# Performance work log

Hardware: AMD Instinct MI355X
Metric: run time of the kernel (lower is better)

The kernel has to match this reference:

```python
import jax, jax.numpy as jnp
import numpy as np

B, S, D = 4, 2048, 1024
H, DH = 16, 64  # dim_q = dim_k = D // H
DFF = 4096


def setup_inputs() -> dict:
    key = jax.random.key(0)
    ks = jax.random.split(key, 12)
    sd = 0.02
    x = jax.random.normal(ks[0], (B, S, D), dtype=jnp.float32)
    mask = jax.random.randint(ks[1], (B, S, S), 0, 2) == 1  # True = masked
    Wq = jax.random.normal(ks[2], (H, D, DH), dtype=jnp.float32) * sd
    bq = jnp.zeros((H, DH), dtype=jnp.float32)
    Wk = jax.random.normal(ks[3], (H, D, DH), dtype=jnp.float32) * sd
    bk = jnp.zeros((H, DH), dtype=jnp.float32)
    Wv = jax.random.normal(ks[4], (H, D, DH), dtype=jnp.float32) * sd
    bv = jnp.zeros((H, DH), dtype=jnp.float32)
    Wo = jax.random.normal(ks[5], (H * DH, D), dtype=jnp.float32) * sd
    bo = jnp.zeros((D,), dtype=jnp.float32)
    W1 = jax.random.normal(ks[6], (D, DFF), dtype=jnp.float32) * sd
    b1 = jnp.zeros((DFF,), dtype=jnp.float32)
    W2 = jax.random.normal(ks[7], (DFF, D), dtype=jnp.float32) * sd
    b2 = jnp.zeros((D,), dtype=jnp.float32)
    return dict(x=x, mask=mask, Wq=Wq, bq=bq, Wk=Wk, bk=bk, Wv=Wv, bv=bv,
                Wo=Wo, bo=bo, W1=W1, b1=b1, W2=W2, b2=b2)


def reference(x, mask, Wq, bq, Wk, bk, Wv, bv, Wo, bo, W1, b1, W2, b2):
    # x: [B,S,D]; mask: [B,S,S] bool (True -> masked)
    # Per-head projections, batched over heads: [B,H,S,DH]
    q = jnp.einsum('bsd,hde->bhse', x, Wq) + bq[None, :, None, :]
    k = jnp.einsum('bsd,hde->bhse', x, Wk) + bk[None, :, None, :]
    v = jnp.einsum('bsd,hde->bhse', x, Wv) + bv[None, :, None, :]
    # NOTE: source scales by sqrt(seq_len) (query.size(1)), reproduced faithfully.
    scale = x.shape[1] ** 0.5
    scores = jnp.einsum('bhse,bhte->bhst', q, k) / scale  # [B,H,S,S]
    scores = jnp.where(mask[:, None, :, :], -1e9, scores)
    attn = jax.nn.softmax(scores, axis=-1)
    ctx = jnp.einsum('bhst,bhte->bhse', attn, v)  # [B,H,S,DH]
    # concat heads -> [B,S,H*DH], output projection
    ctx = jnp.transpose(ctx, (0, 2, 1, 3)).reshape(x.shape[0], x.shape[1], -1)
    out = ctx @ Wo + bo
    # FFN (no residual/LayerNorm in source; dropout = identity in eval)
    h = jax.nn.relu(out @ W1 + b1)
    return h @ W2 + b2
```

## Files before the change

### kernel.cpp

```cpp
#include <hip/hip_runtime.h>
#include <hip/hip_bf16.h>


#define SDIM 2048
#define DDIM 1024

using floatx4 = __attribute__((ext_vector_type(4))) float;
using bf16x8  = __attribute__((ext_vector_type(8))) __bf16;
using bf16x4  = __attribute__((ext_vector_type(4))) __bf16;
using short4v = __attribute__((ext_vector_type(4))) short;

#define GLDS16(gptr, lptr)                                                        \
    __builtin_amdgcn_global_load_lds(                                             \
        (const __attribute__((address_space(1))) void*)(uintptr_t)(gptr),         \
        (__attribute__((address_space(3))) void*)(uintptr_t)(lptr), 16, 0, 0)


__global__ void k_f2b(const float* __restrict__ in, __bf16* __restrict__ out) {
    long i = ((long)blockIdx.x * 256 + threadIdx.x) * 4;
    float4 f = *(const float4*)(in + i);
    bf16x4 v;
    v[0] = (__bf16)f.x; v[1] = (__bf16)f.y; v[2] = (__bf16)f.z; v[3] = (__bf16)f.w;
    *(bf16x4*)(out + i) = v;
}

__global__ void k_tr(const float* __restrict__ in, __bf16* __restrict__ out, int R, int C) {
    __shared__ float t[32][33];
    int nrt = R >> 5;
    int tr = blockIdx.x % nrt, tc = blockIdx.x / nrt;
    int r0 = tr * 32, c0 = tc * 32;
    int lx = threadIdx.x & 31, ly = threadIdx.x >> 5;
    #pragma unroll
    for (int i = 0; i < 32; i += 8) t[ly + i][lx] = in[(long)(r0 + ly + i) * C + c0 + lx];
    __syncthreads();
    #pragma unroll
    for (int i = 0; i < 32; i += 8) out[(long)(c0 + ly + i) * R + r0 + lx] = (__bf16)t[lx][ly + i];
}

__global__ void k_pack_qkvw(const float* __restrict__ Wq, const float* __restrict__ Wk,
                            const float* __restrict__ Wv, __bf16* __restrict__ out) {
    int bid = blockIdx.x;
    int dht = bid & 1;
    int dt = (bid >> 1) & 31;
    int h = (bid >> 6) & 15;
    int which = bid >> 10;
    const float* W = (which == 0) ? Wq : (which == 1) ? Wk : Wv;
    __shared__ float t[32][33];
    int lx = threadIdx.x & 31, ly = threadIdx.x >> 5;
    const float* src = W + ((long)h * 1024 + dt * 32) * 64 + dht * 32;
    #pragma unroll
    for (int i = 0; i < 32; i += 8) t[ly + i][lx] = src[(ly + i) * 64 + lx];
    __syncthreads();
    __bf16* dst = out + ((long)(which * 1024 + h * 64 + dht * 32)) * 1024 + dt * 32;
    #pragma unroll
    for (int i = 0; i < 32; i += 8) dst[(long)(ly + i) * 1024 + lx] = (__bf16)t[lx][ly + i];
}

__global__ void k_pack_qkvb(const float* bq, const float* bk, const float* bv, float* out) {
    int i = blockIdx.x * 256 + threadIdx.x;
    if (i < 3072) {
        int which = i >> 10, r = i & 1023;
        const float* s = (which == 0) ? bq : (which == 1) ? bk : bv;
        out[i] = s[r];
    }
}

__global__ void k_probe(const unsigned* __restrict__ m, int* flag) {
    __shared__ int bad;
    if (threadIdx.x == 0) bad = 0;
    __syncthreads();
    int local = 0;
    for (int i = 0; i < 64; i++) {
        unsigned w = m[threadIdx.x + 256 * i];
        if (w != 0u && w != 1u && w != 0x3f800000u) local = 1;
    }
    if (local) atomicOr(&bad, 1);
    __syncthreads();
    if (threadIdx.x == 0) *flag = bad ? 0 : 1;
}

__global__ void k_pack_mask(const void* __restrict__ mask, const int* __restrict__ flag,
                            unsigned long long* __restrict__ bits) {
    long wid = ((long)blockIdx.x * 256 + threadIdx.x) >> 6;
    int lane = threadIdx.x & 63;
    long e = wid * 64 + lane;
    bool pred;
    if (*flag) pred = ((const unsigned*)mask)[e] != 0u;
    else       pred = ((const unsigned char*)mask)[e] != 0;
    unsigned long long bal = __ballot(pred);
    if (lane == 0) bits[wid] = bal;
}

__global__ void k_remap(const unsigned* __restrict__ bitsDW, unsigned* __restrict__ out) {
    int t = blockIdx.x * 256 + threadIdx.x;
    int q = t & 3, kt = (t >> 2) & 15, srow = t >> 6;
    uint4 md = *(const uint4*)(bitsDW + (long)srow * 64 + kt * 4);
    unsigned d[4] = {md.x, md.y, md.z, md.w};
    unsigned acc = 0;
    #pragma unroll
    for (int ct = 0; ct < 8; ct++) {
        unsigned nib = (d[ct >> 1] >> (((ct & 1) << 4) + q * 4)) & 0xFu;
        acc |= nib << (ct * 4);
    }
    out[srow * 64 + q * 16 + kt] = acc;
}

__global__ void k_trv(const __bf16* __restrict__ Vrow, __bf16* __restrict__ Vt) {
    __shared__ __bf16 t[32][72];
    int p = blockIdx.x >> 6, ts = blockIdx.x & 63;
    int tid = threadIdx.x;
    const __bf16* src = Vrow + ((long)p * 2048 + ts * 32) * 64;
    int s = tid >> 3, c = (tid & 7) * 8;
    *(bf16x8*)&t[s][c] = *(const bf16x8*)&src[s * 64 + c];
    __syncthreads();
    int dh = tid >> 2, sb = (tid & 3) * 8;
    bf16x8 w;
    #pragma unroll
    for (int j = 0; j < 8; j++) w[j] = t[sb + j][dh];
    *(bf16x8*)&Vt[((long)p * 64 + dh) * 2048 + ts * 32 + sb] = w;
}

#define QSZ 8388608L

template <int MODE>
__global__ __launch_bounds__(256, 4) void k_gemm(const __bf16* __restrict__ A,
                                                 const __bf16* __restrict__ Bt,
                                                 const float* __restrict__ bias,
                                                 void* __restrict__ Cout, int Ndim, int K) {
    __shared__ __align__(16) __bf16 As[128 * 64];
    __shared__ __align__(16) __bf16 Bs[128 * 64];
    const int tid = threadIdx.x;
    const int wave = tid >> 6, lane = tid & 63;
    const int q = lane >> 4, l16 = lane & 15;
    const int wr = wave >> 1, wc = wave & 1;
    const long bm = (long)blockIdx.x * 128;
    const long bn = (long)blockIdx.y * 128;
    floatx4 acc[4][4] = {};

    const int srow = lane >> 3;
    const int scol = (((lane & 7) - srow) & 7) * 8;
    const int r8 = l16 & 7;

    const char* apA0 = (const char*)As + (wr * 64 + l16) * 128 + ((q + r8) & 7) * 16;
    const char* apA1 = (const char*)As + (wr * 64 + l16) * 128 + ((q + 4 + r8) & 7) * 16;
    const char* apB0 = (const char*)Bs + (wc * 64 + l16) * 128 + ((q + r8) & 7) * 16;
    const char* apB1 = (const char*)Bs + (wc * 64 + l16) * 128 + ((q + 4 + r8) & 7) * 16;

    for (int k0 = 0; k0 < K; k0 += 64) {
        __syncthreads();
        #pragma unroll
        for (int c = 0; c < 4; c++) {
            int row0 = wave * 32 + c * 8;
            GLDS16(&A[(bm + row0 + srow) * K + k0 + scol], (char*)As + row0 * 128);
            GLDS16(&Bt[(bn + row0 + srow) * K + k0 + scol], (char*)Bs + row0 * 128);
        }
        __syncthreads();
        bf16x8 af[4], bfr[4];
        #pragma unroll
        for (int i = 0; i < 4; i++) af[i] = *(const bf16x8*)(apA0 + i * 2048);
        #pragma unroll
        for (int j = 0; j < 4; j++) bfr[j] = *(const bf16x8*)(apB0 + j * 2048);
        #pragma unroll
        for (int i = 0; i < 4; i++)
            #pragma unroll
            for (int j = 0; j < 4; j++)
                acc[i][j] = __builtin_amdgcn_mfma_f32_16x16x32_bf16(af[i], bfr[j], acc[i][j], 0, 0, 0);
        #pragma unroll
        for (int i = 0; i < 4; i++) af[i] = *(const bf16x8*)(apA1 + i * 2048);
        #pragma unroll
        for (int j = 0; j < 4; j++) bfr[j] = *(const bf16x8*)(apB1 + j * 2048);
        #pragma unroll
        for (int i = 0; i < 4; i++)
            #pragma unroll
            for (int j = 0; j < 4; j++)
                acc[i][j] = __builtin_amdgcn_mfma_f32_16x16x32_bf16(af[i], bfr[j], acc[i][j], 0, 0, 0);
    }

    const int mrow0 = (int)bm + wr * 64 + q * 4;
    const int ncol0 = (int)bn + wc * 64;
    #pragma unroll
    for (int j = 0; j < 4; j++) {
        int nbase = ncol0 + j * 16 + l16;
        float bv = bias[nbase];
        #pragma unroll
        for (int i = 0; i < 4; i++) {
            #pragma unroll
            for (int r = 0; r < 4; r++) {
                int mm = mrow0 + i * 16 + r;
                float v = acc[i][j][r] + bv;
                ((__bf16*)Cout)[(long)mm * Ndim + nbase] = (__bf16)v;
            }
        }
    }
}

template <int MODE, int MREP>
__global__ __launch_bounds__(512, 2) void k_gemm2(const __bf16* __restrict__ A,
                                                  const __bf16* __restrict__ Bt,
                                                  const float* __restrict__ bias,
                                                  void* __restrict__ Cout,
                                                  int Ndim, int K, int NBM) {
    constexpr int BM = MREP * 32;
    __shared__ __align__(16) __bf16 As[2 * BM * 64];
    __shared__ __align__(16) __bf16 Bs[2 * 256 * 64];
    const int tid = threadIdx.x;
    const int wave = tid >> 6, lane = tid & 63;
    const int q = lane >> 4, l16 = lane & 15;
    const int wr = wave >> 2, wc = wave & 3;
    const int nwg = gridDim.x;
    const int id = blockIdx.x;
    const int swz = (id & 7) * (nwg >> 3) + (id >> 3);
    const long bm = (long)(swz % NBM) * BM;
    const long bn = (long)(swz / NBM) * 256;
    floatx4 acc[MREP][4] = {};

    const int s = tid >> 3;
    const int j8 = tid & 7;
    const int sc = ((j8 - s) & 7) * 8;
    const int r8 = l16 & 7;

    const char* apA0 = (const char*)As + (wr * (BM / 2) + l16) * 128 + ((q + r8) & 7) * 16;
    const char* apA1 = (const char*)As + (wr * (BM / 2) + l16) * 128 + ((q + 4 + r8) & 7) * 16;
    const char* apB0 = (const char*)Bs + (wc * 64 + l16) * 128 + ((q + r8) & 7) * 16;
    const char* apB1 = (const char*)Bs + (wc * 64 + l16) * 128 + ((q + 4 + r8) & 7) * 16;

    auto stage = [&](int t, int bsel) __attribute__((always_inline)) {
        const long k0 = (long)t * 64;
        #pragma unroll
        for (int c = 0; c < BM / 64; c++)
            GLDS16(&A[(bm + c * 64 + s) * K + k0 + sc],
                   (char*)As + bsel * (BM * 128) + (c * 64 + wave * 8) * 128);
        #pragma unroll
        for (int c = 0; c < 4; c++)
            GLDS16(&Bt[(bn + c * 64 + s) * K + k0 + sc],
                   (char*)Bs + bsel * 32768 + (c * 64 + wave * 8) * 128);
    };

    auto computeT = [&](int bo) __attribute__((always_inline)) {
        const int oA = bo * (BM * 128);
        const int oB = bo * 32768;
        bf16x8 af[MREP], bfr[4];
        #pragma unroll
        for (int i = 0; i < MREP; i++) af[i] = *(const bf16x8*)(apA0 + oA + i * 2048);
        #pragma unroll
        for (int j = 0; j < 4; j++) bfr[j] = *(const bf16x8*)(apB0 + oB + j * 2048);
        __builtin_amdgcn_s_setprio(1);
        #pragma unroll
        for (int i = 0; i < MREP; i++)
            #pragma unroll
            for (int j = 0; j < 4; j++)
                acc[i][j] = __builtin_amdgcn_mfma_f32_16x16x32_bf16(af[i], bfr[j], acc[i][j], 0, 0, 0);
        __builtin_amdgcn_s_setprio(0);
        #pragma unroll
        for (int i = 0; i < MREP; i++) af[i] = *(const bf16x8*)(apA1 + oA + i * 2048);
        #pragma unroll
        for (int j = 0; j < 4; j++) bfr[j] = *(const bf16x8*)(apB1 + oB + j * 2048);
        __builtin_amdgcn_s_setprio(1);
        #pragma unroll
        for (int i = 0; i < MREP; i++)
            #pragma unroll
            for (int j = 0; j < 4; j++)
                acc[i][j] = __builtin_amdgcn_mfma_f32_16x16x32_bf16(af[i], bfr[j], acc[i][j], 0, 0, 0);
        __builtin_amdgcn_s_setprio(0);
    };

    #define WAITB()                                                                          \
        do {                                                                                 \
            if constexpr (MREP == 8) asm volatile("s_waitcnt vmcnt(8)\n\ts_barrier" ::: "memory"); \
            else                     asm volatile("s_waitcnt vmcnt(6)\n\ts_barrier" ::: "memory"); \
        } while (0)

    const int NT = K >> 6;
    stage(0, 0);
    #pragma unroll 1
    for (int t = 0; t < NT - 2; t += 2) {
        stage(t + 1, 1);
        WAITB();
        computeT(0);
        asm volatile("s_barrier" ::: "memory");
        stage(t + 2, 0);
        WAITB();
        computeT(1);
        asm volatile("s_barrier" ::: "memory");
    }
    stage(NT - 1, 1);
    WAITB();
    computeT(0);
    asm volatile("s_barrier" ::: "memory");
    asm volatile("s_waitcnt vmcnt(0)\n\ts_barrier" ::: "memory");
    computeT(1);
    #undef WAITB

    const int mrow0 = (int)bm + wr * (BM / 2) + q * 4;
    const int ncol0 = (int)bn + wc * 64;
    #pragma unroll
    for (int j = 0; j < 4; j++) {
        int nbase = ncol0 + j * 16 + l16;
        float bv = bias[nbase];
        #pragma unroll
        for (int i = 0; i < MREP; i++) {
            #pragma unroll
            for (int r = 0; r < 4; r++) {
                int mm = mrow0 + i * 16 + r;
                float v = acc[i][j][r] + bv;
                if (MODE == 2) v = fmaxf(v, 0.f);
                if (MODE == 3) {
                    ((float*)Cout)[(long)mm * Ndim + nbase] = v;
                } else if (MODE == 0) {
                    int which = nbase >> 10, rem = nbase & 1023;
                    int hh = rem >> 6, dh = rem & 63;
                    int bb = mm >> 11, ss = mm & 2047;
                    long pr = (long)(bb * 16 + hh);
                    __bf16* o = (__bf16*)Cout;
                    if (which == 0) {
                        v *= 0.03188152837f;
                        o[(pr * 2048 + ss) * 64 + dh] = (__bf16)v;
                    } else if (which == 1) o[QSZ + (pr * 2048 + ss) * 64 + dh] = (__bf16)v;
                    else o[3 * QSZ + (pr * 2048 + ss) * 64 + dh] = (__bf16)v;
                } else {
                    ((__bf16*)Cout)[(long)mm * Ndim + nbase] = (__bf16)v;
                }
            }
        }
    }
}

__global__ __launch_bounds__(256, 2) void k_attn(const __bf16* __restrict__ Q,
                                                 const __bf16* __restrict__ Kb,
                                                 const __bf16* __restrict__ Vt,
                                                 const unsigned* __restrict__ bitw2,
                                                 __bf16* __restrict__ ctx) {
    __shared__ __align__(16) __bf16 Qs[128 * 64];
    __shared__ __align__(16) __bf16 Ks[2][128 * 64];
    __shared__ __align__(16) __bf16 Vts[2][64 * 128];
    const int tid = threadIdx.x, wave = tid >> 6, lane = tid & 63;
    const int q = lane >> 4, l16 = lane & 15;
    const int pair = blockIdx.x & 63, qt = blockIdx.x >> 6;
    const int b = pair >> 4, h = pair & 15;

    const int srow8 = lane >> 3;
    const int scol8 = (((lane & 7) - srow8) & 7) * 8;
    const int r8 = l16 & 7;
    const int vrow = lane >> 4;
    const int vl = lane & 15;

    const char* kp0 = (const char*)Ks + l16 * 128 + ((q + r8) & 7) * 16;
    const char* kp1 = (const char*)Ks + l16 * 128 + ((q + 4 + r8) & 7) * 16;
    const char* vp[8];
    #pragma unroll
    for (int ct = 0; ct < 8; ct++)
        vp[ct] = (const char*)Vts + l16 * 256 + (q & 1) * 8 + ((ct * 2 + (q >> 1) + l16) & 15) * 16;
    const int qrow = qt * 128 + wave * 32 + l16;
    const unsigned* mp0 = bitw2 + ((long)(b * SDIM + qrow)) * 64 + q * 16;
    const unsigned* mp1 = mp0 + 16 * 64;

    floatx4 o[2][4] = {};
    floatx4 o5[2] = {};
    short4v ones;
    { union { unsigned u[2]; short4v s; } c; c.u[0] = 0x3F803F80u; c.u[1] = 0x3F803F80u; ones = c.s; }

    auto stage_kv = [&](int kt, int bufsel) __attribute__((always_inline)) {
        const __bf16* Kp = Kb + ((long)pair * SDIM + kt * 128) * 64;
        #pragma unroll
        for (int c = 0; c < 4; c++) {
            int row0 = wave * 32 + c * 8;
            GLDS16(&Kp[(row0 + srow8) * 64 + scol8], (char*)Ks + bufsel * 16384 + row0 * 128);
        }
        const __bf16* Vp = Vt + ((long)pair * 64) * SDIM + kt * 128;
        #pragma unroll
        for (int c = 0; c < 4; c++) {
            int row0 = wave * 16 + c * 4;
            int gsrc = ((vl - (c * 4 + vrow)) & 15) * 8;
            GLDS16(&Vp[(long)(row0 + vrow) * SDIM + gsrc], (char*)Vts + bufsel * 16384 + row0 * 256);
        }
    };

    const __bf16* Qp = Q + ((long)pair * SDIM + qt * 128) * 64;
    #pragma unroll
    for (int c = 0; c < 4; c++) {
        int row0 = wave * 32 + c * 8;
        GLDS16(&Qp[(row0 + srow8) * 64 + scol8], (char*)Qs + row0 * 128);
    }
    unsigned waA = mp0[0], wbA = mp1[0];
    stage_kv(0, 0);
    asm volatile("s_waitcnt vmcnt(8)\n\ts_barrier" ::: "memory");

    bf16x8 qf[2][2];
    #pragma unroll
    for (int g = 0; g < 2; g++) {
        const char* qb = (const char*)Qs + (wave * 32 + g * 16 + l16) * 128;
        qf[g][0] = *(const bf16x8*)(qb + ((q + r8) & 7) * 16);
        qf[g][1] = *(const bf16x8*)(qb + ((q + 4 + r8) & 7) * 16);
    }

    auto compute = [&](int off, unsigned w32a, unsigned w32b) __attribute__((always_inline)) {
        __builtin_amdgcn_s_setprio(1);
        floatx4 st0[8], st1[8];
        #pragma unroll
        for (int ct = 0; ct < 8; ct++) {
            bf16x8 kf0 = *(const bf16x8*)(kp0 + off + ct * 2048);
            bf16x8 kf1 = *(const bf16x8*)(kp1 + off + ct * 2048);
            floatx4 z0 = {}, z1 = {};
            z0 = __builtin_amdgcn_mfma_f32_16x16x32_bf16(kf0, qf[0][0], z0, 0, 0, 0);
            z1 = __builtin_amdgcn_mfma_f32_16x16x32_bf16(kf0, qf[1][0], z1, 0, 0, 0);
            z0 = __builtin_amdgcn_mfma_f32_16x16x32_bf16(kf1, qf[0][1], z0, 0, 0, 0);
            z1 = __builtin_amdgcn_mfma_f32_16x16x32_bf16(kf1, qf[1][1], z1, 0, 0, 0);
            st0[ct] = z0; st1[ct] = z1;
        }
        #pragma unroll
        for (int ct = 0; ct < 8; ct++) {
            union { unsigned u[2]; short4v s; } pu0, pu1;
            {
                float p0 = __builtin_amdgcn_exp2f(st0[ct][0]);
                float p1 = __builtin_amdgcn_exp2f(st0[ct][1]);
                float p2 = __builtin_amdgcn_exp2f(st0[ct][2]);
                float p3 = __builtin_amdgcn_exp2f(st0[ct][3]);
                p0 = (w32a & (1u << (ct * 4 + 0))) ? 0.f : p0;
                p1 = (w32a & (1u << (ct * 4 + 1))) ? 0.f : p1;
                p2 = (w32a & (1u << (ct * 4 + 2))) ? 0.f : p2;
                p3 = (w32a & (1u << (ct * 4 + 3))) ? 0.f : p3;
                union { float f; unsigned u; } c0, c1, c2, c3;
                c0.f = p0; c1.f = p1; c2.f = p2; c3.f = p3;
                pu0.u[0] = __builtin_amdgcn_perm(c1.u, c0.u, 0x07060302u);
                pu0.u[1] = __builtin_amdgcn_perm(c3.u, c2.u, 0x07060302u);
            }
            {
                float p0 = __builtin_amdgcn_exp2f(st1[ct][0]);
                float p1 = __builtin_amdgcn_exp2f(st1[ct][1]);
                float p2 = __builtin_amdgcn_exp2f(st1[ct][2]);
                float p3 = __builtin_amdgcn_exp2f(st1[ct][3]);
                p0 = (w32b & (1u << (ct * 4 + 0))) ? 0.f : p0;
                p1 = (w32b & (1u << (ct * 4 + 1))) ? 0.f : p1;
                p2 = (w32b & (1u << (ct * 4 + 2))) ? 0.f : p2;
                p3 = (w32b & (1u << (ct * 4 + 3))) ? 0.f : p3;
                union { float f; unsigned u; } c0, c1, c2, c3;
                c0.f = p0; c1.f = p1; c2.f = p2; c3.f = p3;
                pu1.u[0] = __builtin_amdgcn_perm(c1.u, c0.u, 0x07060302u);
                pu1.u[1] = __builtin_amdgcn_perm(c3.u, c2.u, 0x07060302u);
            }
            #pragma unroll
            for (int d = 0; d < 4; d++) {
                union { bf16x4 b; short4v s; } vu;
                vu.b = *(const bf16x4*)(vp[ct] + off + d * 4096);
                o[0][d] = __builtin_amdgcn_mfma_f32_16x16x16bf16_1k(vu.s, pu0.s, o[0][d], 0, 0, 0);
                o[1][d] = __builtin_amdgcn_mfma_f32_16x16x16bf16_1k(vu.s, pu1.s, o[1][d], 0, 0, 0);
            }
            o5[0] = __builtin_amdgcn_mfma_f32_16x16x16bf16_1k(ones, pu0.s, o5[0], 0, 0, 0);
            o5[1] = __builtin_amdgcn_mfma_f32_16x16x16bf16_1k(ones, pu1.s, o5[1], 0, 0, 0);
        }
        __builtin_amdgcn_s_setprio(0);
    };

    #pragma unroll 1
    for (int kt = 0; kt < 14; kt += 2) {
        unsigned waB = mp0[kt + 1], wbB = mp1[kt + 1];
        stage_kv(kt + 1, 1);
        asm volatile("s_waitcnt vmcnt(10)\n\ts_barrier" ::: "memory");
        compute(0, waA, wbA);
        asm volatile("s_barrier" ::: "memory");
        waA = mp0[kt + 2]; wbA = mp1[kt + 2];
        stage_kv(kt + 2, 0);
        asm volatile("s_waitcnt vmcnt(10)\n\ts_barrier" ::: "memory");
        compute(16384, waB, wbB);
        asm volatile("s_barrier" ::: "memory");
    }
    {
        unsigned waB = mp0[15], wbB = mp1[15];
        stage_kv(15, 1);
        asm volatile("s_waitcnt vmcnt(10)\n\ts_barrier" ::: "memory");
        compute(0, waA, wbA);
        asm volatile("s_barrier" ::: "memory");
        asm volatile("s_waitcnt vmcnt(0)\n\ts_barrier" ::: "memory");
        compute(16384, waB, wbB);
    }

    #pragma unroll
    for (int g = 0; g < 2; g++) {
        float inv = 1.0f / o5[g][0];
        long base = ((long)b * SDIM + qrow + g * 16) * DDIM + h * 64;
        #pragma unroll
        for (int d = 0; d < 4; d++) {
            bf16x4 w;
            #pragma unroll
            for (int r = 0; r < 4; r++) w[r] = (__bf16)(o[g][d][r] * inv);
            *(bf16x4*)&ctx[base + d * 16 + q * 4] = w;
        }
    }
}


extern "C" void kernel_launch(void* const* d_in, const int* in_sizes, int n_in,
                              void* d_out, int out_size, void* d_ws, size_t ws_size,
                              hipStream_t stream) {
    const float* x = (const float*)d_in[0];
    const void* mask = d_in[1];
    const float* Wq = (const float*)d_in[2];
    const float* bq = (const float*)d_in[3];
    const float* Wk = (const float*)d_in[4];
    const float* bk = (const float*)d_in[5];
    const float* Wv = (const float*)d_in[6];
    const float* bv = (const float*)d_in[7];
    const float* Wo = (const float*)d_in[8];
    const float* bo = (const float*)d_in[9];
    const float* W1 = (const float*)d_in[10];
    const float* b1 = (const float*)d_in[11];
    const float* W2 = (const float*)d_in[12];
    const float* b2 = (const float*)d_in[13];

    char* ws = (char*)d_ws;
    __bf16* xb   = (__bf16*)(ws + 0);
    __bf16* Qb   = (__bf16*)(ws + 16777216);
    __bf16* Kb   = (__bf16*)(ws + 33554432);
    __bf16* Vtb  = (__bf16*)(ws + 50331648);
    __bf16* Vrow = (__bf16*)(ws + 67108864);
    __bf16* hbuf = (__bf16*)(ws + 33554432);
    __bf16* wqkvt = (__bf16*)(ws + 100663296);
    __bf16* wot  = (__bf16*)(ws + 106954752);
    __bf16* w1t  = (__bf16*)(ws + 109051904);
    __bf16* w2t  = (__bf16*)(ws + 117440512);
    float* bqkv  = (float*)(ws + 125829120);
    int* flag    = (int*)(ws + 125841408);
    __bf16* ctx = xb;
    __bf16* attn_out = Qb;
    unsigned long long* bits = (unsigned long long*)wqkvt;
    unsigned* bits2 = (unsigned*)((char*)wqkvt + 2097152);
    (void)Vrow;

    k_f2b<<<8192, 256, 0, stream>>>(x, xb);
    k_pack_qkvw<<<3072, 256, 0, stream>>>(Wq, Wk, Wv, wqkvt);
    k_pack_qkvb<<<12, 256, 0, stream>>>(bq, bk, bv, bqkv);
    k_tr<<<1024, 256, 0, stream>>>(Wo, wot, 1024, 1024);
    k_tr<<<4096, 256, 0, stream>>>(W1, w1t, 1024, 4096);
    k_tr<<<4096, 256, 0, stream>>>(W2, w2t, 4096, 1024);
    k_probe<<<1, 256, 0, stream>>>((const unsigned*)mask, flag);

    {
        k_gemm2<0, 8><<<384, 512, 0, stream>>>(xb, wqkvt, bqkv, (void*)Qb, 3072, 1024, 32);
    }
    k_trv<<<4096, 256, 0, stream>>>(Vrow, Vtb);
    k_pack_mask<<<65536, 256, 0, stream>>>(mask, flag, bits);
    k_remap<<<2048, 256, 0, stream>>>((const unsigned*)bits, bits2);
    k_attn<<<1024, 256, 0, stream>>>(Qb, Kb, Vtb, bits2, ctx);
    {
        dim3 g(64, 8);
        k_gemm<1><<<g, 256, 0, stream>>>(ctx, wot, bo, (void*)attn_out, 1024, 1024);
    }
    {
        k_gemm2<2, 8><<<512, 512, 0, stream>>>(attn_out, w1t, b1, (void*)hbuf, 4096, 1024, 32);
    }
    {
        k_gemm2<3, 4><<<256, 512, 0, stream>>>(hbuf, w2t, b2, d_out, 1024, 4096, 64);
    }
}
```

Baseline: 611.2 us.

## Replace templated GEMM with triple-buffered 128x256 GEMM and revert QKV to k_gemm

```diff
diff --git a/kernel.cpp b/kernel.cpp
--- a/kernel.cpp
+++ b/kernel.cpp
@@ -184,121 +184,6 @@
         float bv = bias[nbase];
         #pragma unroll
         for (int i = 0; i < 4; i++) {
-            #pragma unroll
-            for (int r = 0; r < 4; r++) {
-                int mm = mrow0 + i * 16 + r;
-                float v = acc[i][j][r] + bv;
-                ((__bf16*)Cout)[(long)mm * Ndim + nbase] = (__bf16)v;
-            }
-        }
-    }
-}
-
-template <int MODE, int MREP>
-__global__ __launch_bounds__(512, 2) void k_gemm2(const __bf16* __restrict__ A,
-                                                  const __bf16* __restrict__ Bt,
-                                                  const float* __restrict__ bias,
-                                                  void* __restrict__ Cout,
-                                                  int Ndim, int K, int NBM) {
-    constexpr int BM = MREP * 32;
-    __shared__ __align__(16) __bf16 As[2 * BM * 64];
-    __shared__ __align__(16) __bf16 Bs[2 * 256 * 64];
-    const int tid = threadIdx.x;
-    const int wave = tid >> 6, lane = tid & 63;
-    const int q = lane >> 4, l16 = lane & 15;
-    const int wr = wave >> 2, wc = wave & 3;
-    const int nwg = gridDim.x;
-    const int id = blockIdx.x;
-    const int swz = (id & 7) * (nwg >> 3) + (id >> 3);
-    const long bm = (long)(swz % NBM) * BM;
-    const long bn = (long)(swz / NBM) * 256;
-    floatx4 acc[MREP][4] = {};
-
-    const int s = tid >> 3;
-    const int j8 = tid & 7;
-    const int sc = ((j8 - s) & 7) * 8;
-    const int r8 = l16 & 7;
-
-    const char* apA0 = (const char*)As + (wr * (BM / 2) + l16) * 128 + ((q + r8) & 7) * 16;
-    const char* apA1 = (const char*)As + (wr * (BM / 2) + l16) * 128 + ((q + 4 + r8) & 7) * 16;
-    const char* apB0 = (const char*)Bs + (wc * 64 + l16) * 128 + ((q + r8) & 7) * 16;
-    const char* apB1 = (const char*)Bs + (wc * 64 + l16) * 128 + ((q + 4 + r8) & 7) * 16;
-
-    auto stage = [&](int t, int bsel) __attribute__((always_inline)) {
-        const long k0 = (long)t * 64;
-        #pragma unroll
-        for (int c = 0; c < BM / 64; c++)
-            GLDS16(&A[(bm + c * 64 + s) * K + k0 + sc],
-                   (char*)As + bsel * (BM * 128) + (c * 64 + wave * 8) * 128);
-        #pragma unroll
-        for (int c = 0; c < 4; c++)
-            GLDS16(&Bt[(bn + c * 64 + s) * K + k0 + sc],
-                   (char*)Bs + bsel * 32768 + (c * 64 + wave * 8) * 128);
-    };
-
-    auto computeT = [&](int bo) __attribute__((always_inline)) {
-        const int oA = bo * (BM * 128);
-        const int oB = bo * 32768;
-        bf16x8 af[MREP], bfr[4];
-        #pragma unroll
-        for (int i = 0; i < MREP; i++) af[i] = *(const bf16x8*)(apA0 + oA + i * 2048);
-        #pragma unroll
-        for (int j = 0; j < 4; j++) bfr[j] = *(const bf16x8*)(apB0 + oB + j * 2048);
-        __builtin_amdgcn_s_setprio(1);
-        #pragma unroll
-        for (int i = 0; i < MREP; i++)
-            #pragma unroll
-            for (int j = 0; j < 4; j++)
-                acc[i][j] = __builtin_amdgcn_mfma_f32_16x16x32_bf16(af[i], bfr[j], acc[i][j], 0, 0, 0);
-        __builtin_amdgcn_s_setprio(0);
-        #pragma unroll
-        for (int i = 0; i < MREP; i++) af[i] = *(const bf16x8*)(apA1 + oA + i * 2048);
-        #pragma unroll
-        for (int j = 0; j < 4; j++) bfr[j] = *(const bf16x8*)(apB1 + oB + j * 2048);
-        __builtin_amdgcn_s_setprio(1);
-        #pragma unroll
-        for (int i = 0; i < MREP; i++)
-            #pragma unroll
-            for (int j = 0; j < 4; j++)
-                acc[i][j] = __builtin_amdgcn_mfma_f32_16x16x32_bf16(af[i], bfr[j], acc[i][j], 0, 0, 0);
-        __builtin_amdgcn_s_setprio(0);
-    };
-
-    #define WAITB()                                                                          \
-        do {                                                                                 \
-            if constexpr (MREP == 8) asm volatile("s_waitcnt vmcnt(8)\n\ts_barrier" ::: "memory"); \
-            else                     asm volatile("s_waitcnt vmcnt(6)\n\ts_barrier" ::: "memory"); \
-        } while (0)
-
-    const int NT = K >> 6;
-    stage(0, 0);
-    #pragma unroll 1
-    for (int t = 0; t < NT - 2; t += 2) {
-        stage(t + 1, 1);
-        WAITB();
-        computeT(0);
-        asm volatile("s_barrier" ::: "memory");
-        stage(t + 2, 0);
-        WAITB();
-        computeT(1);
-        asm volatile("s_barrier" ::: "memory");
-    }
-    stage(NT - 1, 1);
-    WAITB();
-    computeT(0);
-    asm volatile("s_barrier" ::: "memory");
-    asm volatile("s_waitcnt vmcnt(0)\n\ts_barrier" ::: "memory");
-    computeT(1);
-    #undef WAITB
-
-    const int mrow0 = (int)bm + wr * (BM / 2) + q * 4;
-    const int ncol0 = (int)bn + wc * 64;
-    #pragma unroll
-    for (int j = 0; j < 4; j++) {
-        int nbase = ncol0 + j * 16 + l16;
-        float bv = bias[nbase];
-        #pragma unroll
-        for (int i = 0; i < MREP; i++) {
             #pragma unroll
             for (int r = 0; r < 4; r++) {
                 int mm = mrow0 + i * 16 + r;
@@ -317,6 +202,111 @@
                         o[(pr * 2048 + ss) * 64 + dh] = (__bf16)v;
                     } else if (which == 1) o[QSZ + (pr * 2048 + ss) * 64 + dh] = (__bf16)v;
                     else o[3 * QSZ + (pr * 2048 + ss) * 64 + dh] = (__bf16)v;
+                } else {
+                    ((__bf16*)Cout)[(long)mm * Ndim + nbase] = (__bf16)v;
+                }
+            }
+        }
+    }
+}
+
+template <int MODE>
+__global__ __launch_bounds__(512, 2) void k_gemm8(const __bf16* __restrict__ A,
+                                                  const __bf16* __restrict__ Bt,
+                                                  const float* __restrict__ bias,
+                                                  void* __restrict__ Cout,
+                                                  int Ndim, int K, int NBM) {
+    __shared__ __align__(16) __bf16 As[3 * 128 * 64];
+    __shared__ __align__(16) __bf16 Bs[3 * 256 * 64];
+    const int tid = threadIdx.x;
+    const int wave = tid >> 6, lane = tid & 63;
+    const int q = lane >> 4, l16 = lane & 15;
+    const int wr = wave >> 2, wc = wave & 3;
+    const int nwg = gridDim.x;
+    const int id = blockIdx.x;
+    const int swz = (id & 7) * (nwg >> 3) + (id >> 3);
+    const long bm = (long)(swz % NBM) * 128;
+    const long bn = (long)(swz / NBM) * 256;
+    floatx4 acc[4][4] = {};
+
+    const int s = tid >> 3;
+    const int j8 = tid & 7;
+    const int sc = ((j8 - s) & 7) * 8;
+    const int r8 = l16 & 7;
+
+    const char* apA0 = (const char*)As + (wr * 64 + l16) * 128 + ((q + r8) & 7) * 16;
+    const char* apA1 = (const char*)As + (wr * 64 + l16) * 128 + ((q + 4 + r8) & 7) * 16;
+    const char* apB0 = (const char*)Bs + (wc * 64 + l16) * 128 + ((q + r8) & 7) * 16;
+    const char* apB1 = (const char*)Bs + (wc * 64 + l16) * 128 + ((q + 4 + r8) & 7) * 16;
+
+    auto stageA = [&](int t, int r) __attribute__((always_inline)) {
+        const long k0 = (long)t * 64;
+        #pragma unroll
+        for (int c = 0; c < 2; c++)
+            GLDS16(&A[(bm + c * 64 + s) * K + k0 + sc],
+                   (char*)As + r * 16384 + (c * 64 + wave * 8) * 128);
+    };
+    auto stageB = [&](int t, int r) __attribute__((always_inline)) {
+        const long k0 = (long)t * 64;
+        #pragma unroll
+        for (int c = 0; c < 4; c++)
+            GLDS16(&Bt[(bn + c * 64 + s) * K + k0 + sc],
+                   (char*)Bs + r * 32768 + (c * 64 + wave * 8) * 128);
+    };
+
+    stageA(0, 0); stageB(0, 0);
+    stageA(1, 1); stageB(1, 1);
+
+    const int NT = K >> 6;
+    #pragma unroll 1
+    for (int t = 0; t < NT; ++t) {
+        if (t < NT - 1) asm volatile("s_waitcnt vmcnt(6)\n\ts_barrier" ::: "memory");
+        else            asm volatile("s_waitcnt vmcnt(0)\n\ts_barrier" ::: "memory");
+        const int r = t % 3, r2 = (t + 2) % 3;
+        const int oA = r * 16384, oB = r * 32768;
+        const bool st = (t + 2) < NT;
+        bf16x8 af[4], bfr[4];
+        #pragma unroll
+        for (int i = 0; i < 4; i++) af[i] = *(const bf16x8*)(apA0 + oA + i * 2048);
+        #pragma unroll
+        for (int j = 0; j < 4; j++) bfr[j] = *(const bf16x8*)(apB0 + oB + j * 2048);
+        if (st) stageA(t + 2, r2);
+        __builtin_amdgcn_s_setprio(1);
+        #pragma unroll
+        for (int i = 0; i < 4; i++)
+            #pragma unroll
+            for (int j = 0; j < 4; j++)
+                acc[i][j] = __builtin_amdgcn_mfma_f32_16x16x32_bf16(af[i], bfr[j], acc[i][j], 0, 0, 0);
+        __builtin_amdgcn_s_setprio(0);
+        #pragma unroll
+        for (int i = 0; i < 4; i++) af[i] = *(const bf16x8*)(apA1 + oA + i * 2048);
+        #pragma unroll
+        for (int j = 0; j < 4; j++) bfr[j] = *(const bf16x8*)(apB1 + oB + j * 2048);
+        if (st) stageB(t + 2, r2);
+        __builtin_amdgcn_s_setprio(1);
+        #pragma unroll
+        for (int i = 0; i < 4; i++)
+            #pragma unroll
+            for (int j = 0; j < 4; j++)
+                acc[i][j] = __builtin_amdgcn_mfma_f32_16x16x32_bf16(af[i], bfr[j], acc[i][j], 0, 0, 0);
+        __builtin_amdgcn_s_setprio(0);
+    }
+
+    const int mrow0 = (int)bm + wr * 64 + q * 4;
+    const int ncol0 = (int)bn + wc * 64;
+    #pragma unroll
+    for (int j = 0; j < 4; j++) {
+        int nbase = ncol0 + j * 16 + l16;
+        float bv = bias[nbase];
+        #pragma unroll
+        for (int i = 0; i < 4; i++) {
+            #pragma unroll
+            for (int r = 0; r < 4; r++) {
+                int mm = mrow0 + i * 16 + r;
+                float v = acc[i][j][r] + bv;
+                if (MODE == 2) v = fmaxf(v, 0.f);
+                if (MODE == 3) {
+                    ((float*)Cout)[(long)mm * Ndim + nbase] = v;
                 } else {
                     ((__bf16*)Cout)[(long)mm * Ndim + nbase] = (__bf16)v;
                 }
@@ -535,7 +525,8 @@
     k_probe<<<1, 256, 0, stream>>>((const unsigned*)mask, flag);
 
     {
-        k_gemm2<0, 8><<<384, 512, 0, stream>>>(xb, wqkvt, bqkv, (void*)Qb, 3072, 1024, 32);
+        dim3 g(64, 24);
+        k_gemm<0><<<g, 256, 0, stream>>>(xb, wqkvt, bqkv, (void*)Qb, 3072, 1024);
     }
     k_trv<<<4096, 256, 0, stream>>>(Vrow, Vtb);
     k_pack_mask<<<65536, 256, 0, stream>>>(mask, flag, bits);
@@ -546,9 +537,9 @@
         k_gemm<1><<<g, 256, 0, stream>>>(ctx, wot, bo, (void*)attn_out, 1024, 1024);
     }
     {
-        k_gemm2<2, 8><<<512, 512, 0, stream>>>(attn_out, w1t, b1, (void*)hbuf, 4096, 1024, 32);
+        k_gemm8<2><<<1024, 512, 0, stream>>>(attn_out, w1t, b1, (void*)hbuf, 4096, 1024, 64);
     }
     {
-        k_gemm2<3, 4><<<256, 512, 0, stream>>>(hbuf, w2t, b2, d_out, 1024, 4096, 64);
-    }
-}
+        k_gemm8<3><<<256, 512, 0, stream>>>(hbuf, w2t, b2, d_out, 1024, 4096, 64);
+    }
+}
```

Measured after the change: 597.0 us. 1.02x faster.
